# Optimization experiments

Measured on AMD Instinct MI355X. Metric: run time of the kernel, lower is better.

## Reference

```python
import jax, jax.numpy as jnp
import numpy as np

DG = 8   # deformable_groups
KK = 9   # 3x3 kernel
NEG_SLOPE = 0.2


def conv3x3(x, w, b):
    y = jax.lax.conv_general_dilated(x, w, (1, 1), ((1, 1), (1, 1)),
                                     dimension_numbers=('NCHW', 'OIHW', 'NCHW'))
    return y + b[None, :, None, None]


def deform_sample(x, oy, ox, mask):
    # x: [B,C,H,W]; oy/ox/mask: [B,DG,KK,H,W] -> sampled [B,DG,cpg,KK,H,W]
    B, C, H, W = x.shape
    cpg = C // DG
    ky, kx = jnp.meshgrid(jnp.arange(3), jnp.arange(3), indexing='ij')
    ky = (ky.reshape(-1) - 1).astype(x.dtype)  # dilation=1, padding=1
    kx = (kx.reshape(-1) - 1).astype(x.dtype)
    hh = jnp.arange(H, dtype=x.dtype)
    ww = jnp.arange(W, dtype=x.dtype)
    py = hh[None, None, None, :, None] + ky[None, None, :, None, None] + oy
    px = ww[None, None, None, None, :] + kx[None, None, :, None, None] + ox
    y0 = jnp.floor(py)
    x0 = jnp.floor(px)
    fy = py - y0
    fx = px - x0
    xg = x.reshape(B, DG, cpg, H * W)

    def gather(yi, xi):
        valid = ((yi >= 0) & (yi < H) & (xi >= 0) & (xi < W)).astype(x.dtype)
        yc = jnp.clip(yi, 0, H - 1)
        xc = jnp.clip(xi, 0, W - 1)
        idx = (yc * W + xc).reshape(B, DG, 1, KK * H * W)
        v = jnp.take_along_axis(xg, idx, axis=3).reshape(B, DG, cpg, KK, H, W)
        return v * valid[:, :, None]

    y0i = y0.astype(jnp.int32)
    x0i = x0.astype(jnp.int32)
    v00 = gather(y0i, x0i)
    v01 = gather(y0i, x0i + 1)
    v10 = gather(y0i + 1, x0i)
    v11 = gather(y0i + 1, x0i + 1)
    wy = fy[:, :, None]
    wx = fx[:, :, None]
    val = (v00 * (1 - wy) * (1 - wx) + v01 * (1 - wy) * wx
           + v10 * wy * (1 - wx) + v11 * wy * wx)
    return val * mask[:, :, None]


def reference(x, offset, w_off, b_off, w_dcn, b_dcn, w_conv1, b_conv1):
    B, C, H, W = x.shape
    om = conv3x3(offset, w_off, b_off)  # [B, 3*DG*KK, H, W]
    o1, o2, m = jnp.split(om, 3, axis=1)
    oy = o1.reshape(B, DG, KK, H, W)
    ox = o2.reshape(B, DG, KK, H, W)
    mask = jax.nn.sigmoid(m).reshape(B, DG, KK, H, W)
    sampled = deform_sample(x, oy, ox, mask)  # [B,DG,cpg,KK,H,W]
    wd = w_dcn.reshape(w_dcn.shape[0], DG, C // DG, KK)
    dcn = jnp.einsum('bgckhw,ogck->bohw', sampled, wd) + b_dcn[None, :, None, None]
    fea = jnp.where(dcn >= 0, dcn, NEG_SLOPE * dcn)  # LeakyReLU(0.2)
    out = conv3x3(fea, w_conv1, b_conv1) + x  # residual
    return out


def setup_inputs() -> dict:
    key = jax.random.key(0)
    ks = jax.random.split(key, 8)
    B, C, H, W = 4, 64, 96, 96
    offC = 64
    s = 1.0 / np.sqrt(C * 9)
    return {
        'x': jax.random.normal(ks[0], (B, C, H, W), jnp.float32),
        'offset': jax.random.normal(ks[1], (B, offC, H, W), jnp.float32),
        'w_off': jax.random.normal(ks[2], (3 * DG * KK, offC, 3, 3), jnp.float32) * 0.05,
        'b_off': jnp.zeros((3 * DG * KK,), jnp.float32),
        'w_dcn': jax.random.normal(ks[3], (C, C, 3, 3), jnp.float32) * s,
        'b_dcn': jnp.zeros((C,), jnp.float32),
        'w_conv1': jax.random.normal(ks[4], (C, C, 3, 3), jnp.float32) * s,
        'b_conv1': jnp.zeros((C,), jnp.float32),
    }
```

## Files before the change

### kernel.cpp

```cpp
#include <hip/hip_runtime.h>
#include <math.h>

#define HH 96
#define WW 96
#define NB 4
#define NC 64
#define HW (HH*WW)

typedef unsigned short u16;
typedef unsigned int   u32;
typedef __attribute__((ext_vector_type(8))) short bf16x8;
typedef __attribute__((ext_vector_type(4))) float f32x4;

__device__ inline float bf2f(u16 v) { u32 u = ((u32)v) << 16; return __uint_as_float(u); }
__device__ inline u16 f2bf(float f) {
    u32 u = __float_as_uint(f);
    return (u16)((u + 0x7FFFu + ((u >> 16) & 1u)) >> 16);
}
__device__ __forceinline__ float elemf(const u32* a, int i) {
    u32 v = a[i >> 1];
    v = (i & 1) ? (v & 0xFFFF0000u) : (v << 16);
    return __uint_as_float(v);
}

__global__ __launch_bounds__(256) void k_prep(
    const float* __restrict__ x, const float* __restrict__ offset,
    const float* __restrict__ w_off, const float* __restrict__ w_dcn,
    const float* __restrict__ w_c1,
    u16* __restrict__ xt, u16* __restrict__ ot,
    u16* __restrict__ d_off, u16* __restrict__ d_dcn, u16* __restrict__ d_c1) {
    int bx = blockIdx.x;
    int tid = threadIdx.x;
    if (bx < 288) {
        const float* src = (bx < 144) ? x : offset;
        u16* dst = (bx < 144) ? xt : ot;
        int pix = (bx % 144) * 256 + tid;
        int b = pix / HW, hw = pix % HW;
        const float* s = src + b * 64 * HW + hw;
        uint4* dp = (uint4*)(dst + pix * 64);
#pragma unroll
        for (int q = 0; q < 8; ++q) {
            u32 a0 = (u32)f2bf(s[(q*8+0)*HW]) | ((u32)f2bf(s[(q*8+1)*HW]) << 16);
            u32 a1 = (u32)f2bf(s[(q*8+2)*HW]) | ((u32)f2bf(s[(q*8+3)*HW]) << 16);
            u32 a2 = (u32)f2bf(s[(q*8+4)*HW]) | ((u32)f2bf(s[(q*8+5)*HW]) << 16);
            u32 a3 = (u32)f2bf(s[(q*8+6)*HW]) | ((u32)f2bf(s[(q*8+7)*HW]) << 16);
            dp[q] = make_uint4(a0, a1, a2, a3);
        }
        return;
    }
    int rel = bx - 288;
    int m, i0;
    if (rel < 576)      { m = 0; i0 = rel * 256; }
    else if (rel < 720) { m = 1; i0 = (rel - 576) * 256; }
    else                { m = 2; i0 = (rel - 720) * 256; }
    const float* w = (m == 0) ? w_off : ((m == 1) ? w_dcn : w_c1);
    u16* dst = (m == 0) ? d_off : ((m == 1) ? d_dcn : d_c1);
    int NT   = (m == 0) ? 16 : 4;
    int NCO  = (m == 0) ? 216 : 64;
    int i = i0 + tid;
    if (i >= 18 * NT * 512) return;
    int j = i & 7, L = (i >> 3) & 63;
    int cot = (i >> 9) % NT, t = (i >> 9) / NT;
    int k = t * 32 + ((L >> 4) << 3) + j;
    int co = cot * 16 + (L & 15);
    float v = 0.f;
    if (co < NCO) {
        int ci, q;
        if (m == 1) { int c = k & 7, gk = k >> 3; int kk = gk % 9, g = gk / 9; ci = g*8+c; q = kk; }
        else        { q = k >> 6; ci = k & 63; }
        v = w[co * 576 + ci * 9 + q];
    }
    dst[i] = f2bf(v);
}

__global__ __launch_bounds__(256) void k_gemm_off(
    const u16* __restrict__ ot, const u16* __restrict__ wtb,
    const float* __restrict__ bias, u16* __restrict__ omr) {
    __shared__ u16 lb[2 * 8192];
    int tid = threadIdx.x;
    int wid = tid >> 6, L = tid & 63, lr = L & 15, lk = L >> 4;
    int pixblk = blockIdx.x * 64;
    int b = pixblk / HW;
    int yv[4], xv[4];
#pragma unroll
    for (int ms = 0; ms < 4; ++ms) {
        int hw = (pixblk + ms * 16 + lr) % HW;
        yv[ms] = hw / WW; xv[ms] = hw % WW;
    }

    f32x4 acc[4][4];
#pragma unroll
    for (int ms = 0; ms < 4; ++ms)
#pragma unroll
        for (int ct = 0; ct < 4; ++ct) acc[ms][ct] = (f32x4){0.f, 0.f, 0.f, 0.f};

    uint4 rg[4];
    {
        const uint4* s = (const uint4*)wtb;
#pragma unroll
        for (int i = 0; i < 4; ++i) rg[i] = s[tid + i * 256];
        uint4* d = (uint4*)lb;
#pragma unroll
        for (int i = 0; i < 4; ++i) d[tid + i * 256] = rg[i];
    }
    __syncthreads();

    for (int t = 0; t < 18; ++t) {
        if (t + 1 < 18) {
            const uint4* s = (const uint4*)(wtb + (t + 1) * 8192);
#pragma unroll
            for (int i = 0; i < 4; ++i) rg[i] = s[tid + i * 256];
        }
        int q = t >> 1;
        int c0 = (t & 1) * 32 + lk * 8;
        int dy = q / 3 - 1, dx = q % 3 - 1;
        const u16* buf = lb + (t & 1) * 8192;
        bf16x8 bfr[4];
#pragma unroll
        for (int ct = 0; ct < 4; ++ct)
            bfr[ct] = *(const bf16x8*)(buf + ((wid * 4 + ct) * 64 + L) * 8);
#pragma unroll
        for (int ms = 0; ms < 4; ++ms) {
            int yy = yv[ms] + dy, xx = xv[ms] + dx;
            bf16x8 a = {0,0,0,0,0,0,0,0};
            if (yy >= 0 && yy < HH && xx >= 0 && xx < WW)
                a = *(const bf16x8*)(ot + ((b * HH + yy) * WW + xx) * 64 + c0);
#pragma unroll
            for (int ct = 0; ct < 4; ++ct)
                acc[ms][ct] = __builtin_amdgcn_mfma_f32_16x16x32_bf16(a, bfr[ct], acc[ms][ct], 0, 0, 0);
        }
        if (t + 1 < 18) {
            uint4* d = (uint4*)(lb + ((t + 1) & 1) * 8192);
#pragma unroll
            for (int i = 0; i < 4; ++i) d[tid + i * 256] = rg[i];
            __syncthreads();
        }
    }

#pragma unroll
    for (int ms = 0; ms < 4; ++ms) {
        int pixC = pixblk + ms * 16 + lk * 4;
#pragma unroll
        for (int ct = 0; ct < 4; ++ct) {
            int co = (wid * 4 + ct) * 16 + lr;
            if (co < 216) {
                int cls = co / 72;
                int c   = co % 72;
                int g   = c / 9, kk = c % 9;
                int slot = g * 32 + cls * 9 + kk;
                float bs = bias[co];
#pragma unroll
                for (int r = 0; r < 4; ++r) {
                    float v = acc[ms][ct][r] + bs;
                    if (cls == 2) v = 1.f / (1.f + __expf(-v));
                    omr[(pixC + r) * 256 + slot] = f2bf(v);
                }
            }
        }
    }
}

__global__ __launch_bounds__(256) void k_sdcn(
    const u16* __restrict__ xt, const u16* __restrict__ omr,
    const u16* __restrict__ wtb, const float* __restrict__ bias,
    u16* __restrict__ fea) {
    __shared__ u16 sv[32 * 576];
    int tid = threadIdx.x;
    int pixblk = blockIdx.x * 32;
    int p = tid >> 3, g = tid & 7;
    int pix = pixblk + p;
    int b = pixblk / HW;
    int hw = pix % HW, h = hw / WW, w = hw % WW;

    {
        const u16* xb = xt + b * HW * 64 + g * 8;
        const uint4* op = (const uint4*)(omr + (size_t)pix * 256 + g * 32);
        uint4 o0 = op[0], o1 = op[1], o2 = op[2], o3 = op[3];
        u32 oa[16] = {o0.x,o0.y,o0.z,o0.w, o1.x,o1.y,o1.z,o1.w,
                      o2.x,o2.y,o2.z,o2.w, o3.x,o3.y,o3.z,o3.w};
#pragma unroll
        for (int kk = 0; kk < 9; ++kk) {
            float oy   = elemf(oa, kk);
            float ox   = elemf(oa, 9 + kk);
            float mask = elemf(oa, 18 + kk);

            float py = (float)(h + kk / 3 - 1) + oy;
            float px = (float)(w + kk % 3 - 1) + ox;
            float y0f = floorf(py), x0f = floorf(px);
            float fy = py - y0f, fx = px - x0f;
            int y0 = (int)y0f, x0 = (int)x0f, y1 = y0 + 1, x1 = x0 + 1;
            int yc0 = min(max(y0, 0), HH-1), yc1 = min(max(y1, 0), HH-1);
            int xc0 = min(max(x0, 0), WW-1), xc1 = min(max(x1, 0), WW-1);
            float u0 = 1.f - fy, u1 = fy, s0 = 1.f - fx, s1 = fx;
            float w00 = (y0 >= 0 && y0 < HH && x0 >= 0 && x0 < WW) ? u0*s0*mask : 0.f;
            float w01 = (y0 >= 0 && y0 < HH && x1 >= 0 && x1 < WW) ? u0*s1*mask : 0.f;
            float w10 = (y1 >= 0 && y1 < HH && x0 >= 0 && x0 < WW) ? u1*s0*mask : 0.f;
            float w11 = (y1 >= 0 && y1 < HH && x1 >= 0 && x1 < WW) ? u1*s1*mask : 0.f;

            uint4 q00 = *(const uint4*)(xb + (yc0*WW + xc0)*64);
            uint4 q01 = *(const uint4*)(xb + (yc0*WW + xc1)*64);
            uint4 q10 = *(const uint4*)(xb + (yc1*WW + xc0)*64);
            uint4 q11 = *(const uint4*)(xb + (yc1*WW + xc1)*64);

            float r[8];
            {
                float a, bb, c, d;
                a=__uint_as_float(q00.x<<16); bb=__uint_as_float(q01.x<<16); c=__uint_as_float(q10.x<<16); d=__uint_as_float(q11.x<<16);
                r[0]=w00*a+w01*bb+w10*c+w11*d;
                a=__uint_as_float(q00.x&0xFFFF0000u); bb=__uint_as_float(q01.x&0xFFFF0000u); c=__uint_as_float(q10.x&0xFFFF0000u); d=__uint_as_float(q11.x&0xFFFF0000u);
                r[1]=w00*a+w01*bb+w10*c+w11*d;
                a=__uint_as_float(q00.y<<16); bb=__uint_as_float(q01.y<<16); c=__uint_as_float(q10.y<<16); d=__uint_as_float(q11.y<<16);
                r[2]=w00*a+w01*bb+w10*c+w11*d;
                a=__uint_as_float(q00.y&0xFFFF0000u); bb=__uint_as_float(q01.y&0xFFFF0000u); c=__uint_as_float(q10.y&0xFFFF0000u); d=__uint_as_float(q11.y&0xFFFF0000u);
                r[3]=w00*a+w01*bb+w10*c+w11*d;
                a=__uint_as_float(q00.z<<16); bb=__uint_as_float(q01.z<<16); c=__uint_as_float(q10.z<<16); d=__uint_as_float(q11.z<<16);
                r[4]=w00*a+w01*bb+w10*c+w11*d;
                a=__uint_as_float(q00.z&0xFFFF0000u); bb=__uint_as_float(q01.z&0xFFFF0000u); c=__uint_as_float(q10.z&0xFFFF0000u); d=__uint_as_float(q11.z&0xFFFF0000u);
                r[5]=w00*a+w01*bb+w10*c+w11*d;
                a=__uint_as_float(q00.w<<16); bb=__uint_as_float(q01.w<<16); c=__uint_as_float(q10.w<<16); d=__uint_as_float(q11.w<<16);
                r[6]=w00*a+w01*bb+w10*c+w11*d;
                a=__uint_as_float(q00.w&0xFFFF0000u); bb=__uint_as_float(q01.w&0xFFFF0000u); c=__uint_as_float(q10.w&0xFFFF0000u); d=__uint_as_float(q11.w&0xFFFF0000u);
                r[7]=w00*a+w01*bb+w10*c+w11*d;
            }
            u32 a0 = (u32)f2bf(r[0]) | ((u32)f2bf(r[1]) << 16);
            u32 a1 = (u32)f2bf(r[2]) | ((u32)f2bf(r[3]) << 16);
            u32 a2 = (u32)f2bf(r[4]) | ((u32)f2bf(r[5]) << 16);
            u32 a3 = (u32)f2bf(r[6]) | ((u32)f2bf(r[7]) << 16);
            int slot = g * 9 + kk;
            *(uint4*)((char*)sv + p * 1152 + ((slot * 16) ^ ((p & 7) << 4))) = make_uint4(a0, a1, a2, a3);
        }
    }
    __syncthreads();

    int wid = tid >> 6, L = tid & 63, lr = L & 15, lk = L >> 4;
    int pbase = (wid & 1) * 16, cbase = (wid >> 1) * 2;
    int arow = pbase + lr;

    f32x4 acc[2];
    acc[0] = (f32x4){0.f, 0.f, 0.f, 0.f};
    acc[1] = (f32x4){0.f, 0.f, 0.f, 0.f};
#pragma unroll
    for (int t = 0; t < 18; ++t) {
        bf16x8 a = *(const bf16x8*)((const char*)sv + arow * 1152 + (((t * 4 + lk) * 16) ^ ((arow & 7) << 4)));
#pragma unroll
        for (int ct = 0; ct < 2; ++ct) {
            bf16x8 bf = *(const bf16x8*)(wtb + ((t * 4 + cbase + ct) * 64 + L) * 8);
            acc[ct] = __builtin_amdgcn_mfma_f32_16x16x32_bf16(a, bf, acc[ct], 0, 0, 0);
        }
    }
#pragma unroll
    for (int ct = 0; ct < 2; ++ct) {
        int co = (cbase + ct) * 16 + lr;
        float bs = bias[co];
#pragma unroll
        for (int r = 0; r < 4; ++r) {
            float v = acc[ct][r] + bs;
            v = (v >= 0.f) ? v : 0.2f * v;
            fea[(pixblk + pbase + lk * 4 + r) * 64 + co] = f2bf(v);
        }
    }
}

__global__ __launch_bounds__(256) void k_gemm_c1(
    const u16* __restrict__ fea, const u16* __restrict__ wtb,
    const float* __restrict__ bias, const float* __restrict__ xres,
    float* __restrict__ out) {
    __shared__ __align__(16) char smraw[36864];
    u16* lb = (u16*)smraw;
    int tid = threadIdx.x;
    int wid = tid >> 6, L = tid & 63, lr = L & 15, lk = L >> 4;
    int pixblk = blockIdx.x * 64;
    int pixbase = pixblk + wid * 16;
    int pixA = pixbase + lr;
    int b = pixblk / HW;
    int hw = pixA % HW, y = hw / WW, x = hw % WW;

    f32x4 acc[4];
#pragma unroll
    for (int i = 0; i < 4; ++i) acc[i] = (f32x4){0.f, 0.f, 0.f, 0.f};

    {
        const uint4* s = (const uint4*)wtb;
        uint4* d = (uint4*)lb;
#pragma unroll
        for (int i = 0; i < 9; ++i) d[tid + i * 256] = s[tid + i * 256];
    }
    __syncthreads();
    for (int half = 0; half < 2; ++half) {
        int tbase = half * 9;
#pragma unroll
        for (int tl = 0; tl < 9; ++tl) {
            int t = tbase + tl;
            int q = t >> 1;
            int c0 = (t & 1) * 32 + lk * 8;
            int dy = q / 3 - 1, dx = q % 3 - 1;
            int yy = y + dy, xx = x + dx;
            bf16x8 a = {0,0,0,0,0,0,0,0};
            if (yy >= 0 && yy < HH && xx >= 0 && xx < WW)
                a = *(const bf16x8*)(fea + ((b * HH + yy) * WW + xx) * 64 + c0);
            const u16* wp = lb + (tl * 256 + L) * 8;
#pragma unroll
            for (int cot = 0; cot < 4; ++cot) {
                bf16x8 bf = *(const bf16x8*)(wp + cot * 512);
                acc[cot] = __builtin_amdgcn_mfma_f32_16x16x32_bf16(a, bf, acc[cot], 0, 0, 0);
            }
        }
        __syncthreads();
        if (half == 0) {
            const uint4* s = (const uint4*)(wtb + 18432);
            uint4* d = (uint4*)lb;
#pragma unroll
            for (int i = 0; i < 9; ++i) d[tid + i * 256] = s[tid + i * 256];
            __syncthreads();
        }
    }
    float* ob = (float*)smraw;
#pragma unroll
    for (int cot = 0; cot < 4; ++cot) {
#pragma unroll
        for (int r = 0; r < 4; ++r)
            ob[(wid * 16 + lk * 4 + r) * 66 + cot * 16 + lr] = acc[cot][r];
    }
    __syncthreads();
    int p = tid & 63, cg = tid >> 6;
    int hw0 = pixblk % HW;
#pragma unroll
    for (int i = 0; i < 16; ++i) {
        int co = cg * 16 + i;
        int idx = (b * 64 + co) * HW + hw0 + p;
        out[idx] = ob[p * 66 + co] + bias[co] + xres[idx];
    }
}

extern "C" void kernel_launch(void* const* d_in, const int* in_sizes, int n_in,
                              void* d_out, int out_size, void* d_ws, size_t ws_size,
                              hipStream_t stream) {
    const float* x       = (const float*)d_in[0];
    const float* offset  = (const float*)d_in[1];
    const float* w_off   = (const float*)d_in[2];
    const float* b_off   = (const float*)d_in[3];
    const float* w_dcn   = (const float*)d_in[4];
    const float* b_dcn   = (const float*)d_in[5];
    const float* w_conv1 = (const float*)d_in[6];
    const float* b_conv1 = (const float*)d_in[7];
    float* out = (float*)d_out;

    char* ws = (char*)d_ws;
    u16* omr     = (u16*)(ws);
    u16* xt      = (u16*)(ws + 18874368);
    u16* ot      = (u16*)(ws + 23592960);
    u16* fea     = (u16*)(ws + 28311552);
    u16* wtb_off = (u16*)(ws + 33030144);
    u16* wtb_dcn = (u16*)(ws + 33325056);
    u16* wtb_c1  = (u16*)(ws + 33398784);

    hipLaunchKernelGGL(k_prep, dim3(1152), dim3(256), 0, stream,
                       x, offset, w_off, w_dcn, w_conv1, xt, ot, wtb_off, wtb_dcn, wtb_c1);
    hipLaunchKernelGGL(k_gemm_off, dim3(576), dim3(256), 0, stream, ot, wtb_off, b_off, omr);
    hipLaunchKernelGGL(k_sdcn, dim3(1152), dim3(256), 0, stream, xt, omr, wtb_dcn, b_dcn, fea);
    hipLaunchKernelGGL(k_gemm_c1, dim3(576), dim3(256), 0, stream, fea, wtb_c1, b_conv1, x, out);
}
```

Baseline: 184.0 us.

## Split offset-conv GEMM across output-channel halves and load weights directly

```diff
diff --git a/kernel.cpp b/kernel.cpp
--- a/kernel.cpp
+++ b/kernel.cpp
@@ -76,11 +76,13 @@
 __global__ __launch_bounds__(256) void k_gemm_off(
     const u16* __restrict__ ot, const u16* __restrict__ wtb,
     const float* __restrict__ bias, u16* __restrict__ omr) {
-    __shared__ u16 lb[2 * 8192];
     int tid = threadIdx.x;
     int wid = tid >> 6, L = tid & 63, lr = L & 15, lk = L >> 4;
-    int pixblk = blockIdx.x * 64;
+    int bx = blockIdx.x;
+    int mq = bx >> 1, nh = bx & 1;
+    int pixblk = mq * 64;
     int b = pixblk / HW;
+    int cbase = nh * 8 + wid * 2;
     int yv[4], xv[4];
 #pragma unroll
     for (int ms = 0; ms < 4; ++ms) {
@@ -88,52 +90,28 @@
         yv[ms] = hw / WW; xv[ms] = hw % WW;
     }
 
-    f32x4 acc[4][4];
-#pragma unroll
-    for (int ms = 0; ms < 4; ++ms)
-#pragma unroll
-        for (int ct = 0; ct < 4; ++ct) acc[ms][ct] = (f32x4){0.f, 0.f, 0.f, 0.f};
-
-    uint4 rg[4];
-    {
-        const uint4* s = (const uint4*)wtb;
-#pragma unroll
-        for (int i = 0; i < 4; ++i) rg[i] = s[tid + i * 256];
-        uint4* d = (uint4*)lb;
-#pragma unroll
-        for (int i = 0; i < 4; ++i) d[tid + i * 256] = rg[i];
-    }
-    __syncthreads();
-
+    f32x4 acc[4][2];
+#pragma unroll
+    for (int ms = 0; ms < 4; ++ms) {
+        acc[ms][0] = (f32x4){0.f, 0.f, 0.f, 0.f};
+        acc[ms][1] = (f32x4){0.f, 0.f, 0.f, 0.f};
+    }
+
+#pragma unroll 6
     for (int t = 0; t < 18; ++t) {
-        if (t + 1 < 18) {
-            const uint4* s = (const uint4*)(wtb + (t + 1) * 8192);
-#pragma unroll
-            for (int i = 0; i < 4; ++i) rg[i] = s[tid + i * 256];
-        }
         int q = t >> 1;
         int c0 = (t & 1) * 32 + lk * 8;
         int dy = q / 3 - 1, dx = q % 3 - 1;
-        const u16* buf = lb + (t & 1) * 8192;
-        bf16x8 bfr[4];
-#pragma unroll
-        for (int ct = 0; ct < 4; ++ct)
-            bfr[ct] = *(const bf16x8*)(buf + ((wid * 4 + ct) * 64 + L) * 8);
+        bf16x8 b0 = *(const bf16x8*)(wtb + ((t * 16 + cbase + 0) * 64 + L) * 8);
+        bf16x8 b1 = *(const bf16x8*)(wtb + ((t * 16 + cbase + 1) * 64 + L) * 8);
 #pragma unroll
         for (int ms = 0; ms < 4; ++ms) {
             int yy = yv[ms] + dy, xx = xv[ms] + dx;
             bf16x8 a = {0,0,0,0,0,0,0,0};
             if (yy >= 0 && yy < HH && xx >= 0 && xx < WW)
                 a = *(const bf16x8*)(ot + ((b * HH + yy) * WW + xx) * 64 + c0);
-#pragma unroll
-            for (int ct = 0; ct < 4; ++ct)
-                acc[ms][ct] = __builtin_amdgcn_mfma_f32_16x16x32_bf16(a, bfr[ct], acc[ms][ct], 0, 0, 0);
-        }
-        if (t + 1 < 18) {
-            uint4* d = (uint4*)(lb + ((t + 1) & 1) * 8192);
-#pragma unroll
-            for (int i = 0; i < 4; ++i) d[tid + i * 256] = rg[i];
-            __syncthreads();
+            acc[ms][0] = __builtin_amdgcn_mfma_f32_16x16x32_bf16(a, b0, acc[ms][0], 0, 0, 0);
+            acc[ms][1] = __builtin_amdgcn_mfma_f32_16x16x32_bf16(a, b1, acc[ms][1], 0, 0, 0);
         }
     }
 
@@ -141,8 +119,8 @@
     for (int ms = 0; ms < 4; ++ms) {
         int pixC = pixblk + ms * 16 + lk * 4;
 #pragma unroll
-        for (int ct = 0; ct < 4; ++ct) {
-            int co = (wid * 4 + ct) * 16 + lr;
+        for (int ct = 0; ct < 2; ++ct) {
+            int co = (cbase + ct) * 16 + lr;
             if (co < 216) {
                 int cls = co / 72;
                 int c   = co % 72;
@@ -356,7 +334,7 @@
 
     hipLaunchKernelGGL(k_prep, dim3(1152), dim3(256), 0, stream,
                        x, offset, w_off, w_dcn, w_conv1, xt, ot, wtb_off, wtb_dcn, wtb_c1);
-    hipLaunchKernelGGL(k_gemm_off, dim3(576), dim3(256), 0, stream, ot, wtb_off, b_off, omr);
+    hipLaunchKernelGGL(k_gemm_off, dim3(1152), dim3(256), 0, stream, ot, wtb_off, b_off, omr);
     hipLaunchKernelGGL(k_sdcn, dim3(1152), dim3(256), 0, stream, xt, omr, wtb_dcn, b_dcn, fea);
     hipLaunchKernelGGL(k_gemm_c1, dim3(576), dim3(256), 0, stream, fea, wtb_c1, b_conv1, x, out);
 }
```

New measurement: 190.1 us. 1.03x slower.
